# Kernel tuning notes

Hardware: AMD Instinct MI355X
Metric: run time of the kernel (lower is better)

The kernel has to match this reference:

```python
import jax, jax.numpy as jnp
import numpy as np

B, NPB, M, K, F = 4, 8192, 2048, 64, 64   # clouds, points/cloud, fps samples/cloud, max neighbors, feat dim
RADIUS = 0.2
MLP_DIMS = (F + 3, 64, 64, 128)           # local_nn: concat(x_j, pos_j - pos_i) -> 128


def setup_inputs() -> dict:
    key = jax.random.key(0)
    ks = jax.random.split(key, 8)
    N = B * NPB
    x = jax.random.normal(ks[0], (N, F), jnp.float32)
    pos = jax.random.uniform(ks[1], (N, 3), jnp.float32)  # unit cube
    batch = jnp.repeat(jnp.arange(B, dtype=jnp.int32), NPB)
    inp = {"x": x, "pos": pos, "batch": batch}
    for i in range(3):
        din, dout = MLP_DIMS[i], MLP_DIMS[i + 1]
        inp[f"W{i+1}"] = jax.random.normal(ks[2 + i], (din, dout), jnp.float32) / np.sqrt(din)
        inp[f"b{i+1}"] = jnp.zeros((dout,), jnp.float32)
    return inp


def _fps(pos_b):
    """Farthest point sampling on one cloud. pos_b: [n,3] -> [M] indices (start at point 0)."""
    d0 = jnp.sum((pos_b - pos_b[0]) ** 2, axis=-1)  # [n]
    def body(min_d, _):
        idx = jnp.argmax(min_d)
        d = jnp.sum((pos_b - pos_b[idx]) ** 2, axis=-1)
        return jnp.minimum(min_d, d), idx
    _, idxs = jax.lax.scan(body, d0, None, length=M - 1)
    return jnp.concatenate([jnp.zeros((1,), idxs.dtype), idxs])


def _sa_one_cloud(x_b, pos_b, W1, b1, W2, b2, W3, b3):
    samp = _fps(pos_b)                 # [M]
    pos_s = pos_b[samp]                # [M,3]
    # radius-ball query, capped at K nearest inside the ball (centers are in pos so self is always hit)
    d2 = jnp.sum((pos_s[:, None, :] - pos_b[None, :, :]) ** 2, axis=-1)  # [M,n]
    score = jnp.where(d2 <= RADIUS * RADIUS, -d2, -jnp.inf)
    vals, nbr = jax.lax.top_k(score, K)            # [M,K]
    valid = jnp.isfinite(vals)                     # [M,K]
    # PointConv message: MLP(concat(x_j, pos_j - pos_i)), then max-pool over neighbors
    feat = jnp.concatenate([x_b[nbr], pos_b[nbr] - pos_s[:, None, :]], axis=-1)  # [M,K,F+3]
    h = jax.nn.relu(feat @ W1 + b1)
    h = jax.nn.relu(h @ W2 + b2)
    h = jax.nn.relu(h @ W3 + b3)                   # [M,K,128]
    h = jnp.where(valid[:, :, None], h, -jnp.inf)
    return jnp.max(h, axis=1), samp                # [M,128], [M]


def reference(x, pos, batch, W1, b1, W2, b2, W3, b3):
    xb = x.reshape(B, NPB, F)
    pb = pos.reshape(B, NPB, 3)
    out, samp = jax.vmap(lambda xx, pp: _sa_one_cloud(xx, pp, W1, b1, W2, b2, W3, b3))(xb, pb)
    pos_out = jnp.take_along_axis(pb, samp[:, :, None], axis=1)       # [B,M,3]
    batch_out = jnp.repeat(jnp.arange(B, dtype=batch.dtype), M)       # [B*M]
    return out.reshape(B * M, -1), pos_out.reshape(B * M, 3), batch_out
```

## Files before the change

### kernel.cpp

```cpp
#include <hip/hip_runtime.h>

typedef unsigned int u32;
typedef unsigned long long u64;
typedef float f32x2 __attribute__((ext_vector_type(2)));

#define NPB 8192
#define BCL 4
#define MS 2048
#define KN 64
#define TOTC (BCL * MS)
#define OFF_POS   (BCL * MS * 128)
#define OFF_BATCH (OFF_POS + BCL * MS * 3)
#define SMEM_BYTES (NPB * 16 + 32 + MS * 4)
#define GRP_PRIV 40208
#define CONS_BLKS ((TOTC + 2) / 3)

__device__ inline u64 umax64(u64 a, u64 b) { return a < b ? b : a; }
__device__ inline u32 umax32(u32 a, u32 b) { return a < b ? b : a; }

__device__ inline f32x2 pk_add(f32x2 a, f32x2 b) {
  f32x2 d;
  asm("v_pk_add_f32 %0, %1, %2" : "=v"(d) : "v"(a), "v"(b));
  return d;
}
__device__ inline f32x2 pk_mul(f32x2 a, f32x2 b) {
  f32x2 d;
  asm("v_pk_mul_f32 %0, %1, %2" : "=v"(d) : "v"(a), "v"(b));
  return d;
}

__device__ inline u32 wave_max_u32(u32 v) {
  v = umax32(v, (u32)__builtin_amdgcn_update_dpp(0, (int)v, 0x111, 0xf, 0xf, false));
  v = umax32(v, (u32)__builtin_amdgcn_update_dpp(0, (int)v, 0x112, 0xf, 0xf, false));
  v = umax32(v, (u32)__builtin_amdgcn_update_dpp(0, (int)v, 0x114, 0xf, 0xf, false));
  v = umax32(v, (u32)__builtin_amdgcn_update_dpp(0, (int)v, 0x118, 0xf, 0xf, false));
  v = umax32(v, (u32)__builtin_amdgcn_update_dpp(0, (int)v, 0x142, 0xa, 0xf, false));
  v = umax32(v, (u32)__builtin_amdgcn_update_dpp(0, (int)v, 0x143, 0xc, 0xf, false));
  return (u32)__builtin_amdgcn_readlane((int)v, 63);
}
__device__ inline u64 wave_max_key(u64 lkey) {
  u32 hi = (u32)(lkey >> 32), lo32v = (u32)lkey;
  u32 m = wave_max_u32(hi);
  u32 c = wave_max_u32(hi == m ? lo32v : 0u);
  return ((u64)m << 32) | c;
}

__device__ inline u32 part1by2(u32 x) {
  x &= 0x3ffu;
  x = (x | (x << 16)) & 0x030000FFu;
  x = (x | (x << 8))  & 0x0300F00Fu;
  x = (x | (x << 4))  & 0x030C30C3u;
  x = (x | (x << 2))  & 0x09249249u;
  return x;
}

__global__ __launch_bounds__(1024) void init_ready(u32* __restrict__ ready) {
  int i = blockIdx.x * 1024 + threadIdx.x;
  if (i < TOTC) ready[i] = 0u;
}

__global__ __launch_bounds__(1024) void pipeline_kernel(
    const float* __restrict__ x, const float* __restrict__ pos,
    u32* __restrict__ ready,
    const float* __restrict__ W1, const float* __restrict__ b1,
    const float* __restrict__ W2, const float* __restrict__ b2,
    const float* __restrict__ W3, const float* __restrict__ b3,
    float* __restrict__ out) {
  __shared__ __align__(16) unsigned char smem_raw[SMEM_BYTES];
  int t = threadIdx.x;

  if (blockIdx.x < BCL) {
    u64* sortb = (u64*)smem_raw;
    float4* tab = (float4*)smem_raw;
    u64* slot = (u64*)(smem_raw + NPB * 16);
    int* s_samp = (int*)(smem_raw + NPB * 16 + 32);

    int b = blockIdx.x, lane = t & 63;
    const float* pb = pos + (size_t)b * NPB * 3;

    if (t == 1) atomicExch(&ready[(size_t)b * MS], 1u);

    for (int i = t; i < NPB; i += 1024) {
      float xx = pb[i * 3], yy = pb[i * 3 + 1], zz = pb[i * 3 + 2];
      u32 xi = (u32)fminf(fmaxf(xx * 1024.0f, 0.0f), 1023.0f);
      u32 yi = (u32)fminf(fmaxf(yy * 1024.0f, 0.0f), 1023.0f);
      u32 zi = (u32)fminf(fmaxf(zz * 1024.0f, 0.0f), 1023.0f);
      u32 m = (part1by2(zi) << 2) | (part1by2(yi) << 1) | part1by2(xi);
      sortb[i] = ((u64)m << 13) | (u32)i;
    }
    for (int k = 2; k <= NPB; k <<= 1) {
      for (int j = k >> 1; j > 0; j >>= 1) {
        __syncthreads();
        for (int i = t; i < NPB; i += 1024) {
          int ix = i ^ j;
          if (ix > i) {
            u64 a = sortb[i], c = sortb[ix];
            bool up = ((i & k) == 0);
            if ((a > c) == up) { sortb[i] = c; sortb[ix] = a; }
          }
        }
      }
    }
    __syncthreads();
    int oi[8];
    #pragma unroll
    for (int i = 0; i < 8; ++i) oi[i] = (int)(sortb[8 * t + i] & 0x1FFFu);
    __syncthreads();

    for (int i = t; i < NPB; i += 1024) {
      float xx = pb[i * 3], yy = pb[i * 3 + 1], zz = pb[i * 3 + 2];
      tab[i] = float4{xx, yy, zz, 0.0f};
    }
    if (t < 3) slot[t] = 0;
    if (t == 0) s_samp[0] = 0;
    __syncthreads();

    f32x2 px[4], py[4], pz[4], mind[4];
    u32 lo[8];
    float bxl = 1e30f, bxh = -1e30f, byl = 1e30f, byh = -1e30f, bzl = 1e30f, bzh = -1e30f;
    #pragma unroll
    for (int j = 0; j < 4; ++j) {
      int iA = oi[2 * j], iB = oi[2 * j + 1];
      float4 A = tab[iA], B = tab[iB];
      px[j] = f32x2{A.x, B.x}; py[j] = f32x2{A.y, B.y}; pz[j] = f32x2{A.z, B.z};
      lo[2 * j] = ~(u32)iA; lo[2 * j + 1] = ~(u32)iB;
      bxl = fminf(bxl, fminf(A.x, B.x)); bxh = fmaxf(bxh, fmaxf(A.x, B.x));
      byl = fminf(byl, fminf(A.y, B.y)); byh = fmaxf(byh, fmaxf(A.y, B.y));
      bzl = fminf(bzl, fminf(A.z, B.z)); bzh = fmaxf(bzh, fmaxf(A.z, B.z));
    }
    u64 lkey = 0, wkey;
    {
      float4 c0 = tab[0];
      f32x2 mcx = f32x2{-c0.x, -c0.x}, mcy = f32x2{-c0.y, -c0.y}, mcz = f32x2{-c0.z, -c0.z};
      #pragma unroll
      for (int j = 0; j < 4; ++j) {
        f32x2 dx = pk_add(px[j], mcx), dy = pk_add(py[j], mcy), dz = pk_add(pz[j], mcz);
        mind[j] = pk_add(pk_add(pk_mul(dx, dx), pk_mul(dy, dy)), pk_mul(dz, dz));
        u64 kA = ((u64)__float_as_uint(mind[j].x) << 32) | lo[2 * j];
        u64 kB = ((u64)__float_as_uint(mind[j].y) << 32) | lo[2 * j + 1];
        lkey = umax64(lkey, umax64(kA, kB));
      }
      wkey = wave_max_key(lkey);
    }

    int cur = 0, nxt = 1;
    for (int it = 1; it < MS; ++it) {
      if (lane == 0) atomicMax((u64*)&slot[cur], wkey);
      if (t == 64) slot[nxt] = 0;
      __syncthreads();
      u64 g = slot[cur];
      int win = (int)(~(u32)g) & (NPB - 1);
      if (t == 0) s_samp[it] = win;
      if (t == 65) atomicExch(&ready[(size_t)b * MS + it], (u32)(win + 1));
      float4 wc = tab[win];
      float ncx = wc.x, ncy = wc.y, ncz = wc.z;
      float lmax = __uint_as_float((u32)(lkey >> 32));
      float ax = fmaxf(fmaxf(__fsub_rn(bxl, ncx), __fsub_rn(ncx, bxh)), 0.0f);
      float ay = fmaxf(fmaxf(__fsub_rn(byl, ncy), __fsub_rn(ncy, byh)), 0.0f);
      float az = fmaxf(fmaxf(__fsub_rn(bzl, ncz), __fsub_rn(ncz, bzh)), 0.0f);
      float lb2 = (ax * ax + ay * ay + az * az) * 0.9999961853f;
      bool upd = (lb2 <= lmax);
      if (__ballot(upd)) {
        if (upd) {
          f32x2 mcx = f32x2{-ncx, -ncx}, mcy = f32x2{-ncy, -ncy}, mcz = f32x2{-ncz, -ncz};
          u64 acc = 0;
          #pragma unroll
          for (int j = 0; j < 4; ++j) {
            f32x2 dx = pk_add(px[j], mcx), dy = pk_add(py[j], mcy), dz = pk_add(pz[j], mcz);
            f32x2 d2 = pk_add(pk_add(pk_mul(dx, dx), pk_mul(dy, dy)), pk_mul(dz, dz));
            mind[j].x = fminf(mind[j].x, d2.x);
            mind[j].y = fminf(mind[j].y, d2.y);
            u64 kA = ((u64)__float_as_uint(mind[j].x) << 32) | lo[2 * j];
            u64 kB = ((u64)__float_as_uint(mind[j].y) << 32) | lo[2 * j + 1];
            acc = umax64(acc, umax64(kA, kB));
          }
          lkey = acc;
        }
        wkey = wave_max_key(lkey);
      }
      cur = nxt;
      nxt = nxt + 1 == 3 ? 0 : nxt + 1;
    }
    __syncthreads();
    float* pos_out = out + OFF_POS + (size_t)b * MS * 3;
    float* batch_out = out + OFF_BATCH + (size_t)b * MS;
    for (int m = t; m < MS; m += 1024) {
      int s = s_samp[m];
      float4 c = tab[s];
      pos_out[m * 3] = c.x;
      pos_out[m * 3 + 1] = c.y;
      pos_out[m * 3 + 2] = c.z;
      batch_out[m] = (float)b;
    }
    return;
  }

  {
    int cblk = blockIdx.x - BCL;
    int g = t >> 8;
    int tl = t & 255;
    bool work = (g < 3);
    int p = 3 * cblk + (work ? g : 0);
    if (p >= TOTC) p = TOTC - 1;
    int b = p & (BCL - 1), m = p >> 2;
    int c = b * MS + m;
    const float R2CUT = (float)(0.2 * 0.2);

    float (*s_w)[64] = (float(*)[64])(smem_raw);
    unsigned char* gb = smem_raw + 17408 + (work ? g : 0) * GRP_PRIV;
    u64* cand = (u64*)gb;
    int* s_cnt = (int*)(gb + 4096);
    int* s_win = (int*)(gb + 4100);
    float (*s_feat)[68] = (float(*)[68])(gb + 4112);
    float (*s_h)[68]    = (float(*)[68])(gb + 21520);
    float* s_mask       = (float*)(gb + 38928);
    float (*s_red)[64]  = (float(*)[64])(gb + 39184);

    const float* pb = pos + (size_t)b * NPB * 3;

    if (work && tl == 0) {
      u32 v;
      while ((v = atomicAdd(&ready[c], 0u)) == 0u) __builtin_amdgcn_s_sleep(8);
      *s_win = (int)(v - 1u);
      *s_cnt = 0;
    }
    __syncthreads();
    int s = 0;
    float cx = 0.0f, cy = 0.0f, cz = 0.0f;
    if (work) {
      s = *s_win;
      cx = pb[s * 3]; cy = pb[s * 3 + 1]; cz = pb[s * 3 + 2];
    }

    if (work) {
      for (int j = tl; j < NPB; j += 256) {
        float dx = __fsub_rn(pb[j * 3], cx);
        float dy = __fsub_rn(pb[j * 3 + 1], cy);
        float dz = __fsub_rn(pb[j * 3 + 2], cz);
        float d2 = __fadd_rn(__fadd_rn(__fmul_rn(dx, dx), __fmul_rn(dy, dy)), __fmul_rn(dz, dz));
        if (d2 <= R2CUT) {
          int sl = atomicAdd(s_cnt, 1);
          if (sl < 512) cand[sl] = ((u64)__float_as_uint(d2) << 32) | (u32)j;
        }
      }
    }
    __syncthreads();
    int n = 0;
    if (work) {
      n = *s_cnt; if (n > 512) n = 512;
      for (int i = tl; i < 512; i += 256) if (i >= n) cand[i] = ~0ull;
    }
    __syncthreads();
    for (int k = 2; k <= 512; k <<= 1) {
      for (int j = k >> 1; j > 0; j >>= 1) {
        if (work) {
          for (int i = tl; i < 512; i += 256) {
            int ix = i ^ j;
            if (ix > i) {
              u64 a = cand[i], bb = cand[ix];
              bool up = ((i & k) == 0);
              if ((a > bb) == up) { cand[i] = bb; cand[ix] = a; }
            }
          }
        }
        __syncthreads();
      }
    }

    if (work) {
      int r = tl >> 2, q = tl & 3;
      int j = (r < n) ? (int)(cand[r] & 0xffffffffu) : -1;
      bool valid = (j >= 0 && j < NPB);
      size_t jj = valid ? (size_t)j : 0;
      const float4* xp = (const float4*)(x + ((size_t)b * NPB + jj) * 64 + q * 16);
      float4 v[4];
      for (int i = 0; i < 4; ++i) v[i] = xp[i];
      for (int i = 0; i < 4; ++i) {
        s_feat[r][q * 16 + i * 4 + 0] = valid ? v[i].x : 0.0f;
        s_feat[r][q * 16 + i * 4 + 1] = valid ? v[i].y : 0.0f;
        s_feat[r][q * 16 + i * 4 + 2] = valid ? v[i].z : 0.0f;
        s_feat[r][q * 16 + i * 4 + 3] = valid ? v[i].w : 0.0f;
      }
    }
    if (work && tl < 64) {
      int r = tl;
      int j = (r < n) ? (int)(cand[r] & 0xffffffffu) : -1;
      bool valid = (j >= 0 && j < NPB);
      s_mask[r] = valid ? 0.0f : -__builtin_inff();
      size_t jj = valid ? (size_t)j : (size_t)s;
      for (int d = 0; d < 3; ++d) {
        float pj = pos[((size_t)b * NPB + jj) * 3 + d];
        float pc = pos[((size_t)b * NPB + s) * 3 + d];
        s_feat[r][64 + d] = __fsub_rn(pj, pc);
      }
    }
    for (int idx = t; idx < 67 * 64; idx += 1024)
      s_w[idx >> 6][idx & 63] = W1[idx];
    __syncthreads();

    {
      int r = tl >> 2, n0 = (tl & 3) * 16;
      float acc[16];
      if (work) {
        for (int j = 0; j < 16; ++j) acc[j] = b1[n0 + j];
        for (int k = 0; k < 67; ++k) {
          float f = s_feat[r][k];
          for (int j = 0; j < 16; ++j) acc[j] += f * s_w[k][n0 + j];
        }
      }
      __syncthreads();
      if (work) {
        for (int j = 0; j < 16; ++j) s_h[r][n0 + j] = fmaxf(acc[j], 0.0f);
      }
      for (int idx = t; idx < 64 * 64; idx += 1024)
        s_w[idx >> 6][idx & 63] = W2[idx];
    }
    __syncthreads();

    {
      int r = tl >> 2, n0 = (tl & 3) * 16;
      float acc[16];
      if (work) {
        for (int j = 0; j < 16; ++j) acc[j] = b2[n0 + j];
        for (int k = 0; k < 64; ++k) {
          float f = s_h[r][k];
          for (int j = 0; j < 16; ++j) acc[j] += f * s_w[k][n0 + j];
        }
      }
      __syncthreads();
      if (work) {
        for (int j = 0; j < 16; ++j) s_feat[r][n0 + j] = fmaxf(acc[j], 0.0f);
      }
    }
    __syncthreads();

    for (int h = 0; h < 2; ++h) {
      for (int idx = t; idx < 64 * 64; idx += 1024)
        s_w[idx >> 6][idx & 63] = W3[(size_t)(idx >> 6) * 128 + h * 64 + (idx & 63)];
      __syncthreads();
      if (work) {
        int n2 = tl & 63, rg = tl >> 6;
        float acc[16];
        float bias = b3[h * 64 + n2];
        for (int rr = 0; rr < 16; ++rr) acc[rr] = bias;
        for (int k = 0; k < 64; ++k) {
          float w = s_w[k][n2];
          for (int rr = 0; rr < 16; ++rr) acc[rr] += s_feat[rg * 16 + rr][k] * w;
        }
        float mm = -__builtin_inff();
        for (int rr = 0; rr < 16; ++rr)
          mm = fmaxf(mm, fmaxf(acc[rr], 0.0f) + s_mask[rg * 16 + rr]);
        s_red[rg][n2] = mm;
      }
      __syncthreads();
      if (work && tl < 64) {
        float mm = fmaxf(fmaxf(s_red[0][tl], s_red[1][tl]), fmaxf(s_red[2][tl], s_red[3][tl]));
        out[(size_t)c * 128 + h * 64 + tl] = mm;
      }
      __syncthreads();
    }
  }
}

extern "C" void kernel_launch(void* const* d_in, const int* in_sizes, int n_in,
                              void* d_out, int out_size, void* d_ws, size_t ws_size,
                              hipStream_t stream) {
  const float* x   = (const float*)d_in[0];
  const float* pos = (const float*)d_in[1];
  const float* W1 = (const float*)d_in[3];
  const float* b1 = (const float*)d_in[4];
  const float* W2 = (const float*)d_in[5];
  const float* b2 = (const float*)d_in[6];
  const float* W3 = (const float*)d_in[7];
  const float* b3 = (const float*)d_in[8];

  float* out = (float*)d_out;
  u32* ready = (u32*)d_ws;

  init_ready<<<(TOTC + 1023) / 1024, 1024, 0, stream>>>(ready);
  pipeline_kernel<<<BCL + CONS_BLKS, 1024, 0, stream>>>(
      x, pos, ready, W1, b1, W2, b2, W3, b3, out);
}
```

Measured before the change: 1.484 ms.

## Spread FPS argmax atomics over four LDS slots and batch ready-flag publishes

The per-iteration LDS atomicMax used to hit one slot from all 16 waves. It now spreads across four slots that are reduced after the barrier, which cuts same-address atomic serialization on the FPS critical path. The producer also packs four 13-bit sample indices into one 64-bit ready word with a valid bit, so it issues a global atomic only every fourth iteration. In exchange, consumers see samples up to three iterations later, which slightly delays pipeline overlap.

```diff
diff --git a/kernel.cpp b/kernel.cpp
--- a/kernel.cpp
+++ b/kernel.cpp
@@ -11,7 +11,7 @@
 #define TOTC (BCL * MS)
 #define OFF_POS   (BCL * MS * 128)
 #define OFF_BATCH (OFF_POS + BCL * MS * 3)
-#define SMEM_BYTES (NPB * 16 + 32 + MS * 4)
+#define SMEM_BYTES (NPB * 16 + 96 + MS * 4)
 #define GRP_PRIV 40208
 #define CONS_BLKS ((TOTC + 2) / 3)
 
@@ -54,14 +54,14 @@
   return x;
 }
 
-__global__ __launch_bounds__(1024) void init_ready(u32* __restrict__ ready) {
+__global__ __launch_bounds__(1024) void init_ready(u64* __restrict__ ready) {
   int i = blockIdx.x * 1024 + threadIdx.x;
-  if (i < TOTC) ready[i] = 0u;
+  if (i < TOTC / 4) ready[i] = 0ull;
 }
 
 __global__ __launch_bounds__(1024) void pipeline_kernel(
     const float* __restrict__ x, const float* __restrict__ pos,
-    u32* __restrict__ ready,
+    u64* __restrict__ ready,
     const float* __restrict__ W1, const float* __restrict__ b1,
     const float* __restrict__ W2, const float* __restrict__ b2,
     const float* __restrict__ W3, const float* __restrict__ b3,
@@ -72,13 +72,11 @@
   if (blockIdx.x < BCL) {
     u64* sortb = (u64*)smem_raw;
     float4* tab = (float4*)smem_raw;
-    u64* slot = (u64*)(smem_raw + NPB * 16);
-    int* s_samp = (int*)(smem_raw + NPB * 16 + 32);
-
-    int b = blockIdx.x, lane = t & 63;
+    u64 (*slotv)[4] = (u64(*)[4])(smem_raw + NPB * 16);
+    int* s_samp = (int*)(smem_raw + NPB * 16 + 96);
+
+    int b = blockIdx.x, lane = t & 63, wid = t >> 6;
     const float* pb = pos + (size_t)b * NPB * 3;
-
-    if (t == 1) atomicExch(&ready[(size_t)b * MS], 1u);
 
     for (int i = t; i < NPB; i += 1024) {
       float xx = pb[i * 3], yy = pb[i * 3 + 1], zz = pb[i * 3 + 2];
@@ -111,7 +109,7 @@
       float xx = pb[i * 3], yy = pb[i * 3 + 1], zz = pb[i * 3 + 2];
       tab[i] = float4{xx, yy, zz, 0.0f};
     }
-    if (t < 3) slot[t] = 0;
+    if (t < 12) ((u64*)slotv)[t] = 0;
     if (t == 0) s_samp[0] = 0;
     __syncthreads();
 
@@ -143,15 +141,23 @@
       wkey = wave_max_key(lkey);
     }
 
+    u64 pk = 0;
     int cur = 0, nxt = 1;
     for (int it = 1; it < MS; ++it) {
-      if (lane == 0) atomicMax((u64*)&slot[cur], wkey);
-      if (t == 64) slot[nxt] = 0;
-      __syncthreads();
-      u64 g = slot[cur];
+      if (lane == 0) atomicMax(&slotv[cur][wid & 3], wkey);
+      if (t >= 64 && t < 68) slotv[nxt][t - 64] = 0;
+      __syncthreads();
+      ulonglong2 s01 = *(const ulonglong2*)&slotv[cur][0];
+      ulonglong2 s23 = *(const ulonglong2*)&slotv[cur][2];
+      u64 g = umax64(umax64(s01.x, s01.y), umax64(s23.x, s23.y));
       int win = (int)(~(u32)g) & (NPB - 1);
       if (t == 0) s_samp[it] = win;
-      if (t == 65) atomicExch(&ready[(size_t)b * MS + it], (u32)(win + 1));
+      pk = (pk << 13) | (u32)win;
+      if ((it & 3) == 3) {
+        if (t == 65)
+          atomicExch(&ready[(size_t)b * (MS / 4) + (it >> 2)], pk | (1ull << 63));
+        pk = 0;
+      }
       float4 wc = tab[win];
       float ncx = wc.x, ncy = wc.y, ncz = wc.z;
       float lmax = __uint_as_float((u32)(lkey >> 32));
@@ -219,9 +225,11 @@
     const float* pb = pos + (size_t)b * NPB * 3;
 
     if (work && tl == 0) {
-      u32 v;
-      while ((v = atomicAdd(&ready[c], 0u)) == 0u) __builtin_amdgcn_s_sleep(8);
-      *s_win = (int)(v - 1u);
+      int grp = m >> 2, sub = m & 3;
+      u64 v;
+      while (!((v = atomicAdd(&ready[(size_t)b * (MS / 4) + grp], 0ull)) >> 63))
+        __builtin_amdgcn_s_sleep(8);
+      *s_win = (int)((v >> ((3 - sub) * 13)) & (u64)(NPB - 1));
       *s_cnt = 0;
     }
     __syncthreads();
@@ -375,9 +383,9 @@
   const float* b3 = (const float*)d_in[8];
 
   float* out = (float*)d_out;
-  u32* ready = (u32*)d_ws;
-
-  init_ready<<<(TOTC + 1023) / 1024, 1024, 0, stream>>>(ready);
+  u64* ready = (u64*)d_ws;
+
+  init_ready<<<(TOTC / 4 + 1023) / 1024, 1024, 0, stream>>>(ready);
   pipeline_kernel<<<BCL + CONS_BLKS, 1024, 0, stream>>>(
       x, pos, ready, W1, b1, W2, b2, W3, b3, out);
 }
```

Measured after the change: 1.775 ms. +19.6%, slower.

## Map four clouds' centers per consumer block and relax FPS barrier

Applied to the files above, without the earlier changes.

Consumer blocks now handle one sample index across all four clouds, one 256-thread group per cloud, instead of three centers per block with an idle fourth group. Because producers advance all clouds in lockstep, each block's four centers become ready at about the same time. The separate hidden-layer buffer is dropped in favour of writing layer outputs back in place into the feature buffer, which shrinks per-group shared memory so four groups fit. The FPS loop swaps __syncthreads for an explicit lgkmcnt wait plus s_barrier with a scheduling barrier, aiming to cut per-iteration sync cost; this relies on the LDS/scalar waitcnt being enough for correctness.

```diff
diff --git a/kernel.cpp b/kernel.cpp
--- a/kernel.cpp
+++ b/kernel.cpp
@@ -12,8 +12,8 @@
 #define OFF_POS   (BCL * MS * 128)
 #define OFF_BATCH (OFF_POS + BCL * MS * 3)
 #define SMEM_BYTES (NPB * 16 + 32 + MS * 4)
-#define GRP_PRIV 40208
-#define CONS_BLKS ((TOTC + 2) / 3)
+#define GRP_PRIV 22800
+#define CONS_BLKS MS
 
 __device__ inline u64 umax64(u64 a, u64 b) { return a < b ? b : a; }
 __device__ inline u32 umax32(u32 a, u32 b) { return a < b ? b : a; }
@@ -147,7 +147,9 @@
     for (int it = 1; it < MS; ++it) {
       if (lane == 0) atomicMax((u64*)&slot[cur], wkey);
       if (t == 64) slot[nxt] = 0;
-      __syncthreads();
+      asm volatile("s_waitcnt lgkmcnt(0)" ::: "memory");
+      __builtin_amdgcn_s_barrier();
+      __builtin_amdgcn_sched_barrier(0);
       u64 g = slot[cur];
       int win = (int)(~(u32)g) & (NPB - 1);
       if (t == 0) s_samp[it] = win;
@@ -199,75 +201,60 @@
     int cblk = blockIdx.x - BCL;
     int g = t >> 8;
     int tl = t & 255;
-    bool work = (g < 3);
-    int p = 3 * cblk + (work ? g : 0);
-    if (p >= TOTC) p = TOTC - 1;
-    int b = p & (BCL - 1), m = p >> 2;
+    int b = g, m = cblk;
     int c = b * MS + m;
     const float R2CUT = (float)(0.2 * 0.2);
 
     float (*s_w)[64] = (float(*)[64])(smem_raw);
-    unsigned char* gb = smem_raw + 17408 + (work ? g : 0) * GRP_PRIV;
+    unsigned char* gb = smem_raw + 17408 + g * GRP_PRIV;
     u64* cand = (u64*)gb;
     int* s_cnt = (int*)(gb + 4096);
     int* s_win = (int*)(gb + 4100);
     float (*s_feat)[68] = (float(*)[68])(gb + 4112);
-    float (*s_h)[68]    = (float(*)[68])(gb + 21520);
-    float* s_mask       = (float*)(gb + 38928);
-    float (*s_red)[64]  = (float(*)[64])(gb + 39184);
+    float* s_mask       = (float*)(gb + 21520);
+    float (*s_red)[64]  = (float(*)[64])(gb + 21776);
 
     const float* pb = pos + (size_t)b * NPB * 3;
 
-    if (work && tl == 0) {
+    if (tl == 0) {
       u32 v;
       while ((v = atomicAdd(&ready[c], 0u)) == 0u) __builtin_amdgcn_s_sleep(8);
       *s_win = (int)(v - 1u);
       *s_cnt = 0;
     }
     __syncthreads();
-    int s = 0;
-    float cx = 0.0f, cy = 0.0f, cz = 0.0f;
-    if (work) {
-      s = *s_win;
-      cx = pb[s * 3]; cy = pb[s * 3 + 1]; cz = pb[s * 3 + 2];
-    }
-
-    if (work) {
-      for (int j = tl; j < NPB; j += 256) {
-        float dx = __fsub_rn(pb[j * 3], cx);
-        float dy = __fsub_rn(pb[j * 3 + 1], cy);
-        float dz = __fsub_rn(pb[j * 3 + 2], cz);
-        float d2 = __fadd_rn(__fadd_rn(__fmul_rn(dx, dx), __fmul_rn(dy, dy)), __fmul_rn(dz, dz));
-        if (d2 <= R2CUT) {
-          int sl = atomicAdd(s_cnt, 1);
-          if (sl < 512) cand[sl] = ((u64)__float_as_uint(d2) << 32) | (u32)j;
-        }
-      }
-    }
-    __syncthreads();
-    int n = 0;
-    if (work) {
-      n = *s_cnt; if (n > 512) n = 512;
-      for (int i = tl; i < 512; i += 256) if (i >= n) cand[i] = ~0ull;
-    }
+    int s = *s_win;
+    float cx = pb[s * 3], cy = pb[s * 3 + 1], cz = pb[s * 3 + 2];
+
+    for (int j = tl; j < NPB; j += 256) {
+      float dx = __fsub_rn(pb[j * 3], cx);
+      float dy = __fsub_rn(pb[j * 3 + 1], cy);
+      float dz = __fsub_rn(pb[j * 3 + 2], cz);
+      float d2 = __fadd_rn(__fadd_rn(__fmul_rn(dx, dx), __fmul_rn(dy, dy)), __fmul_rn(dz, dz));
+      if (d2 <= R2CUT) {
+        int sl = atomicAdd(s_cnt, 1);
+        if (sl < 512) cand[sl] = ((u64)__float_as_uint(d2) << 32) | (u32)j;
+      }
+    }
+    __syncthreads();
+    int n = *s_cnt; if (n > 512) n = 512;
+    for (int i = tl; i < 512; i += 256) if (i >= n) cand[i] = ~0ull;
     __syncthreads();
     for (int k = 2; k <= 512; k <<= 1) {
       for (int j = k >> 1; j > 0; j >>= 1) {
-        if (work) {
-          for (int i = tl; i < 512; i += 256) {
-            int ix = i ^ j;
-            if (ix > i) {
-              u64 a = cand[i], bb = cand[ix];
-              bool up = ((i & k) == 0);
-              if ((a > bb) == up) { cand[i] = bb; cand[ix] = a; }
-            }
+        for (int i = tl; i < 512; i += 256) {
+          int ix = i ^ j;
+          if (ix > i) {
+            u64 a = cand[i], bb = cand[ix];
+            bool up = ((i & k) == 0);
+            if ((a > bb) == up) { cand[i] = bb; cand[ix] = a; }
           }
         }
         __syncthreads();
       }
     }
 
-    if (work) {
+    {
       int r = tl >> 2, q = tl & 3;
       int j = (r < n) ? (int)(cand[r] & 0xffffffffu) : -1;
       bool valid = (j >= 0 && j < NPB);
@@ -282,7 +269,7 @@
         s_feat[r][q * 16 + i * 4 + 3] = valid ? v[i].w : 0.0f;
       }
     }
-    if (work && tl < 64) {
+    if (tl < 64) {
       int r = tl;
       int j = (r < n) ? (int)(cand[r] & 0xffffffffu) : -1;
       bool valid = (j >= 0 && j < NPB);
@@ -301,17 +288,13 @@
     {
       int r = tl >> 2, n0 = (tl & 3) * 16;
       float acc[16];
-      if (work) {
-        for (int j = 0; j < 16; ++j) acc[j] = b1[n0 + j];
-        for (int k = 0; k < 67; ++k) {
-          float f = s_feat[r][k];
-          for (int j = 0; j < 16; ++j) acc[j] += f * s_w[k][n0 + j];
-        }
-      }
-      __syncthreads();
-      if (work) {
-        for (int j = 0; j < 16; ++j) s_h[r][n0 + j] = fmaxf(acc[j], 0.0f);
-      }
+      for (int j = 0; j < 16; ++j) acc[j] = b1[n0 + j];
+      for (int k = 0; k < 67; ++k) {
+        float f = s_feat[r][k];
+        for (int j = 0; j < 16; ++j) acc[j] += f * s_w[k][n0 + j];
+      }
+      __syncthreads();
+      for (int j = 0; j < 16; ++j) s_feat[r][n0 + j] = fmaxf(acc[j], 0.0f);
       for (int idx = t; idx < 64 * 64; idx += 1024)
         s_w[idx >> 6][idx & 63] = W2[idx];
     }
@@ -320,17 +303,13 @@
     {
       int r = tl >> 2, n0 = (tl & 3) * 16;
       float acc[16];
-      if (work) {
-        for (int j = 0; j < 16; ++j) acc[j] = b2[n0 + j];
-        for (int k = 0; k < 64; ++k) {
-          float f = s_h[r][k];
-          for (int j = 0; j < 16; ++j) acc[j] += f * s_w[k][n0 + j];
-        }
-      }
-      __syncthreads();
-      if (work) {
-        for (int j = 0; j < 16; ++j) s_feat[r][n0 + j] = fmaxf(acc[j], 0.0f);
-      }
+      for (int j = 0; j < 16; ++j) acc[j] = b2[n0 + j];
+      for (int k = 0; k < 64; ++k) {
+        float f = s_feat[r][k];
+        for (int j = 0; j < 16; ++j) acc[j] += f * s_w[k][n0 + j];
+      }
+      __syncthreads();
+      for (int j = 0; j < 16; ++j) s_feat[r][n0 + j] = fmaxf(acc[j], 0.0f);
     }
     __syncthreads();
 
@@ -338,24 +317,22 @@
       for (int idx = t; idx < 64 * 64; idx += 1024)
         s_w[idx >> 6][idx & 63] = W3[(size_t)(idx >> 6) * 128 + h * 64 + (idx & 63)];
       __syncthreads();
-      if (work) {
-        int n2 = tl & 63, rg = tl >> 6;
-        float acc[16];
-        float bias = b3[h * 64 + n2];
-        for (int rr = 0; rr < 16; ++rr) acc[rr] = bias;
-        for (int k = 0; k < 64; ++k) {
-          float w = s_w[k][n2];
-          for (int rr = 0; rr < 16; ++rr) acc[rr] += s_feat[rg * 16 + rr][k] * w;
-        }
-        float mm = -__builtin_inff();
-        for (int rr = 0; rr < 16; ++rr)
-          mm = fmaxf(mm, fmaxf(acc[rr], 0.0f) + s_mask[rg * 16 + rr]);
-        s_red[rg][n2] = mm;
-      }
-      __syncthreads();
-      if (work && tl < 64) {
-        float mm = fmaxf(fmaxf(s_red[0][tl], s_red[1][tl]), fmaxf(s_red[2][tl], s_red[3][tl]));
-        out[(size_t)c * 128 + h * 64 + tl] = mm;
+      int n2 = tl & 63, rg = tl >> 6;
+      float acc[16];
+      float bias = b3[h * 64 + n2];
+      for (int rr = 0; rr < 16; ++rr) acc[rr] = bias;
+      for (int k = 0; k < 64; ++k) {
+        float w = s_w[k][n2];
+        for (int rr = 0; rr < 16; ++rr) acc[rr] += s_feat[rg * 16 + rr][k] * w;
+      }
+      float mm = -__builtin_inff();
+      for (int rr = 0; rr < 16; ++rr)
+        mm = fmaxf(mm, fmaxf(acc[rr], 0.0f) + s_mask[rg * 16 + rr]);
+      s_red[rg][n2] = mm;
+      __syncthreads();
+      if (tl < 64) {
+        float mm2 = fmaxf(fmaxf(s_red[0][tl], s_red[1][tl]), fmaxf(s_red[2][tl], s_red[3][tl]));
+        out[(size_t)c * 128 + h * 64 + tl] = mm2;
       }
       __syncthreads();
     }
```

New measurement: 1.495 ms. Within noise of the previous version (+0.7%).

## Use persistent consumer blocks with cloud positions cached in LDS

Applied to the files above, without the earlier changes.

Consumer blocks become persistent: each block is bound to one cloud, copies that cloud's positions into shared memory once, and loops over 17 centers in a strided slot order, with two working groups per block instead of three. The ball query and relative-position computation now read the LDS copy instead of global memory. The intermediate s_h buffer is dropped in favour of writing back into s_feat, and the FPS barrier becomes a raw s_barrier with an explicit lgkmcnt wait. This is meant to cut repeated global position reads and block launch overhead, but it lowers per-block parallelism and lets consumers sit spinning while they wait on FPS progress.

```diff
diff --git a/kernel.cpp b/kernel.cpp
--- a/kernel.cpp
+++ b/kernel.cpp
@@ -11,9 +11,14 @@
 #define TOTC (BCL * MS)
 #define OFF_POS   (BCL * MS * 128)
 #define OFF_BATCH (OFF_POS + BCL * MS * 3)
-#define SMEM_BYTES (NPB * 16 + 32 + MS * 4)
-#define GRP_PRIV 40208
-#define CONS_BLKS ((TOTC + 2) / 3)
+#define TAB3_B   98304
+#define SW_OFF   98304
+#define GRP_OFF  115712
+#define GRP_PRIV 22800
+#define SMEM_BYTES 161312
+#define CONS_BLKS 252
+#define SLOTS 126
+#define NITER 17
 
 __device__ inline u64 umax64(u64 a, u64 b) { return a < b ? b : a; }
 __device__ inline u32 umax32(u32 a, u32 b) { return a < b ? b : a; }
@@ -147,7 +152,9 @@
     for (int it = 1; it < MS; ++it) {
       if (lane == 0) atomicMax((u64*)&slot[cur], wkey);
       if (t == 64) slot[nxt] = 0;
-      __syncthreads();
+      asm volatile("s_waitcnt lgkmcnt(0)" ::: "memory");
+      __builtin_amdgcn_s_barrier();
+      __builtin_amdgcn_sched_barrier(0);
       u64 g = slot[cur];
       int win = (int)(~(u32)g) & (NPB - 1);
       if (t == 0) s_samp[it] = win;
@@ -196,168 +203,177 @@
   }
 
   {
-    int cblk = blockIdx.x - BCL;
+    int cb = blockIdx.x - BCL;
+    int b = cb & (BCL - 1);
+    int q = cb >> 2;
     int g = t >> 8;
     int tl = t & 255;
-    bool work = (g < 3);
-    int p = 3 * cblk + (work ? g : 0);
-    if (p >= TOTC) p = TOTC - 1;
-    int b = p & (BCL - 1), m = p >> 2;
-    int c = b * MS + m;
+    bool work = (g < 2);
+    int slot = q * 2 + (work ? g : 0);
     const float R2CUT = (float)(0.2 * 0.2);
 
-    float (*s_w)[64] = (float(*)[64])(smem_raw);
-    unsigned char* gb = smem_raw + 17408 + (work ? g : 0) * GRP_PRIV;
+    float* tab3 = (float*)smem_raw;
+    float (*s_w)[64] = (float(*)[64])(smem_raw + SW_OFF);
+    unsigned char* gb = smem_raw + GRP_OFF + (work ? g : 0) * GRP_PRIV;
     u64* cand = (u64*)gb;
     int* s_cnt = (int*)(gb + 4096);
     int* s_win = (int*)(gb + 4100);
     float (*s_feat)[68] = (float(*)[68])(gb + 4112);
-    float (*s_h)[68]    = (float(*)[68])(gb + 21520);
-    float* s_mask       = (float*)(gb + 38928);
-    float (*s_red)[64]  = (float(*)[64])(gb + 39184);
+    float* s_mask       = (float*)(gb + 21520);
+    float (*s_red)[64]  = (float(*)[64])(gb + 21776);
 
     const float* pb = pos + (size_t)b * NPB * 3;
-
-    if (work && tl == 0) {
-      u32 v;
-      while ((v = atomicAdd(&ready[c], 0u)) == 0u) __builtin_amdgcn_s_sleep(8);
-      *s_win = (int)(v - 1u);
-      *s_cnt = 0;
-    }
-    __syncthreads();
-    int s = 0;
-    float cx = 0.0f, cy = 0.0f, cz = 0.0f;
-    if (work) {
-      s = *s_win;
-      cx = pb[s * 3]; cy = pb[s * 3 + 1]; cz = pb[s * 3 + 2];
-    }
-
-    if (work) {
-      for (int j = tl; j < NPB; j += 256) {
-        float dx = __fsub_rn(pb[j * 3], cx);
-        float dy = __fsub_rn(pb[j * 3 + 1], cy);
-        float dz = __fsub_rn(pb[j * 3 + 2], cz);
-        float d2 = __fadd_rn(__fadd_rn(__fmul_rn(dx, dx), __fmul_rn(dy, dy)), __fmul_rn(dz, dz));
-        if (d2 <= R2CUT) {
-          int sl = atomicAdd(s_cnt, 1);
-          if (sl < 512) cand[sl] = ((u64)__float_as_uint(d2) << 32) | (u32)j;
-        }
-      }
-    }
-    __syncthreads();
-    int n = 0;
-    if (work) {
-      n = *s_cnt; if (n > 512) n = 512;
-      for (int i = tl; i < 512; i += 256) if (i >= n) cand[i] = ~0ull;
-    }
-    __syncthreads();
-    for (int k = 2; k <= 512; k <<= 1) {
-      for (int j = k >> 1; j > 0; j >>= 1) {
-        if (work) {
-          for (int i = tl; i < 512; i += 256) {
-            int ix = i ^ j;
-            if (ix > i) {
-              u64 a = cand[i], bb = cand[ix];
-              bool up = ((i & k) == 0);
-              if ((a > bb) == up) { cand[i] = bb; cand[ix] = a; }
+    for (int i = t; i < NPB * 3; i += 1024) tab3[i] = pb[i];
+    __syncthreads();
+
+    for (int k = 0; k < NITER; ++k) {
+      int m = slot + k * SLOTS;
+      if (m >= MS) m = MS - 1;
+      int c = b * MS + m;
+
+      if (work && tl == 0) {
+        u32 v;
+        while ((v = __hip_atomic_load(&ready[c], __ATOMIC_RELAXED,
+                                      __HIP_MEMORY_SCOPE_AGENT)) == 0u)
+          __builtin_amdgcn_s_sleep(32);
+        *s_win = (int)(v - 1u);
+        *s_cnt = 0;
+      }
+      __syncthreads();
+      int s = 0;
+      float cx = 0.0f, cy = 0.0f, cz = 0.0f;
+      if (work) {
+        s = *s_win;
+        cx = tab3[s * 3]; cy = tab3[s * 3 + 1]; cz = tab3[s * 3 + 2];
+      }
+
+      if (work) {
+        for (int j = tl; j < NPB; j += 256) {
+          float dx = __fsub_rn(tab3[j * 3], cx);
+          float dy = __fsub_rn(tab3[j * 3 + 1], cy);
+          float dz = __fsub_rn(tab3[j * 3 + 2], cz);
+          float d2 = __fadd_rn(__fadd_rn(__fmul_rn(dx, dx), __fmul_rn(dy, dy)), __fmul_rn(dz, dz));
+          if (d2 <= R2CUT) {
+            int sl = atomicAdd(s_cnt, 1);
+            if (sl < 512) cand[sl] = ((u64)__float_as_uint(d2) << 32) | (u32)j;
+          }
+        }
+      }
+      __syncthreads();
+      int n = 0;
+      if (work) {
+        n = *s_cnt; if (n > 512) n = 512;
+        for (int i = tl; i < 512; i += 256) if (i >= n) cand[i] = ~0ull;
+      }
+      __syncthreads();
+      for (int kk = 2; kk <= 512; kk <<= 1) {
+        for (int j = kk >> 1; j > 0; j >>= 1) {
+          if (work) {
+            for (int i = tl; i < 512; i += 256) {
+              int ix = i ^ j;
+              if (ix > i) {
+                u64 a = cand[i], bb = cand[ix];
+                bool up = ((i & kk) == 0);
+                if ((a > bb) == up) { cand[i] = bb; cand[ix] = a; }
+              }
             }
           }
-        }
-        __syncthreads();
-      }
-    }
-
-    if (work) {
-      int r = tl >> 2, q = tl & 3;
-      int j = (r < n) ? (int)(cand[r] & 0xffffffffu) : -1;
-      bool valid = (j >= 0 && j < NPB);
-      size_t jj = valid ? (size_t)j : 0;
-      const float4* xp = (const float4*)(x + ((size_t)b * NPB + jj) * 64 + q * 16);
-      float4 v[4];
-      for (int i = 0; i < 4; ++i) v[i] = xp[i];
-      for (int i = 0; i < 4; ++i) {
-        s_feat[r][q * 16 + i * 4 + 0] = valid ? v[i].x : 0.0f;
-        s_feat[r][q * 16 + i * 4 + 1] = valid ? v[i].y : 0.0f;
-        s_feat[r][q * 16 + i * 4 + 2] = valid ? v[i].z : 0.0f;
-        s_feat[r][q * 16 + i * 4 + 3] = valid ? v[i].w : 0.0f;
-      }
-    }
-    if (work && tl < 64) {
-      int r = tl;
-      int j = (r < n) ? (int)(cand[r] & 0xffffffffu) : -1;
-      bool valid = (j >= 0 && j < NPB);
-      s_mask[r] = valid ? 0.0f : -__builtin_inff();
-      size_t jj = valid ? (size_t)j : (size_t)s;
-      for (int d = 0; d < 3; ++d) {
-        float pj = pos[((size_t)b * NPB + jj) * 3 + d];
-        float pc = pos[((size_t)b * NPB + s) * 3 + d];
-        s_feat[r][64 + d] = __fsub_rn(pj, pc);
-      }
-    }
-    for (int idx = t; idx < 67 * 64; idx += 1024)
-      s_w[idx >> 6][idx & 63] = W1[idx];
-    __syncthreads();
-
-    {
-      int r = tl >> 2, n0 = (tl & 3) * 16;
-      float acc[16];
+          __syncthreads();
+        }
+      }
+
       if (work) {
-        for (int j = 0; j < 16; ++j) acc[j] = b1[n0 + j];
-        for (int k = 0; k < 67; ++k) {
-          float f = s_feat[r][k];
-          for (int j = 0; j < 16; ++j) acc[j] += f * s_w[k][n0 + j];
-        }
-      }
-      __syncthreads();
-      if (work) {
-        for (int j = 0; j < 16; ++j) s_h[r][n0 + j] = fmaxf(acc[j], 0.0f);
-      }
-      for (int idx = t; idx < 64 * 64; idx += 1024)
-        s_w[idx >> 6][idx & 63] = W2[idx];
-    }
-    __syncthreads();
-
-    {
-      int r = tl >> 2, n0 = (tl & 3) * 16;
-      float acc[16];
-      if (work) {
-        for (int j = 0; j < 16; ++j) acc[j] = b2[n0 + j];
-        for (int k = 0; k < 64; ++k) {
-          float f = s_h[r][k];
-          for (int j = 0; j < 16; ++j) acc[j] += f * s_w[k][n0 + j];
-        }
-      }
-      __syncthreads();
-      if (work) {
-        for (int j = 0; j < 16; ++j) s_feat[r][n0 + j] = fmaxf(acc[j], 0.0f);
-      }
-    }
-    __syncthreads();
-
-    for (int h = 0; h < 2; ++h) {
-      for (int idx = t; idx < 64 * 64; idx += 1024)
-        s_w[idx >> 6][idx & 63] = W3[(size_t)(idx >> 6) * 128 + h * 64 + (idx & 63)];
-      __syncthreads();
-      if (work) {
-        int n2 = tl & 63, rg = tl >> 6;
+        int r = tl >> 2, qq = tl & 3;
+        int j = (r < n) ? (int)(cand[r] & 0xffffffffu) : -1;
+        bool valid = (j >= 0 && j < NPB);
+        size_t jj = valid ? (size_t)j : 0;
+        const float4* xp = (const float4*)(x + ((size_t)b * NPB + jj) * 64 + qq * 16);
+        float4 v[4];
+        for (int i = 0; i < 4; ++i) v[i] = xp[i];
+        for (int i = 0; i < 4; ++i) {
+          s_feat[r][qq * 16 + i * 4 + 0] = valid ? v[i].x : 0.0f;
+          s_feat[r][qq * 16 + i * 4 + 1] = valid ? v[i].y : 0.0f;
+          s_feat[r][qq * 16 + i * 4 + 2] = valid ? v[i].z : 0.0f;
+          s_feat[r][qq * 16 + i * 4 + 3] = valid ? v[i].w : 0.0f;
+        }
+      }
+      if (work && tl < 64) {
+        int r = tl;
+        int j = (r < n) ? (int)(cand[r] & 0xffffffffu) : -1;
+        bool valid = (j >= 0 && j < NPB);
+        s_mask[r] = valid ? 0.0f : -__builtin_inff();
+        size_t jj = valid ? (size_t)j : (size_t)s;
+        for (int d = 0; d < 3; ++d) {
+          float pj = tab3[jj * 3 + d];
+          float pc = tab3[(size_t)s * 3 + d];
+          s_feat[r][64 + d] = __fsub_rn(pj, pc);
+        }
+      }
+      for (int idx = t; idx < 67 * 64; idx += 1024)
+        s_w[idx >> 6][idx & 63] = W1[idx];
+      __syncthreads();
+
+      {
+        int r = tl >> 2, n0 = (tl & 3) * 16;
         float acc[16];
-        float bias = b3[h * 64 + n2];
-        for (int rr = 0; rr < 16; ++rr) acc[rr] = bias;
-        for (int k = 0; k < 64; ++k) {
-          float w = s_w[k][n2];
-          for (int rr = 0; rr < 16; ++rr) acc[rr] += s_feat[rg * 16 + rr][k] * w;
-        }
-        float mm = -__builtin_inff();
-        for (int rr = 0; rr < 16; ++rr)
-          mm = fmaxf(mm, fmaxf(acc[rr], 0.0f) + s_mask[rg * 16 + rr]);
-        s_red[rg][n2] = mm;
-      }
-      __syncthreads();
-      if (work && tl < 64) {
-        float mm = fmaxf(fmaxf(s_red[0][tl], s_red[1][tl]), fmaxf(s_red[2][tl], s_red[3][tl]));
-        out[(size_t)c * 128 + h * 64 + tl] = mm;
-      }
-      __syncthreads();
+        if (work) {
+          for (int j = 0; j < 16; ++j) acc[j] = b1[n0 + j];
+          for (int kk = 0; kk < 67; ++kk) {
+            float f = s_feat[r][kk];
+            for (int j = 0; j < 16; ++j) acc[j] += f * s_w[kk][n0 + j];
+          }
+        }
+        __syncthreads();
+        if (work) {
+          for (int j = 0; j < 16; ++j) s_feat[r][n0 + j] = fmaxf(acc[j], 0.0f);
+        }
+        for (int idx = t; idx < 64 * 64; idx += 1024)
+          s_w[idx >> 6][idx & 63] = W2[idx];
+      }
+      __syncthreads();
+
+      {
+        int r = tl >> 2, n0 = (tl & 3) * 16;
+        float acc[16];
+        if (work) {
+          for (int j = 0; j < 16; ++j) acc[j] = b2[n0 + j];
+          for (int kk = 0; kk < 64; ++kk) {
+            float f = s_feat[r][kk];
+            for (int j = 0; j < 16; ++j) acc[j] += f * s_w[kk][n0 + j];
+          }
+        }
+        __syncthreads();
+        if (work) {
+          for (int j = 0; j < 16; ++j) s_feat[r][n0 + j] = fmaxf(acc[j], 0.0f);
+        }
+      }
+      __syncthreads();
+
+      for (int h = 0; h < 2; ++h) {
+        for (int idx = t; idx < 64 * 64; idx += 1024)
+          s_w[idx >> 6][idx & 63] = W3[(size_t)(idx >> 6) * 128 + h * 64 + (idx & 63)];
+        __syncthreads();
+        if (work) {
+          int n2 = tl & 63, rg = tl >> 6;
+          float acc[16];
+          float bias = b3[h * 64 + n2];
+          for (int rr = 0; rr < 16; ++rr) acc[rr] = bias;
+          for (int kk = 0; kk < 64; ++kk) {
+            float w = s_w[kk][n2];
+            for (int rr = 0; rr < 16; ++rr) acc[rr] += s_feat[rg * 16 + rr][kk] * w;
+          }
+          float mm = -__builtin_inff();
+          for (int rr = 0; rr < 16; ++rr)
+            mm = fmaxf(mm, fmaxf(acc[rr], 0.0f) + s_mask[rg * 16 + rr]);
+          s_red[rg][n2] = mm;
+        }
+        __syncthreads();
+        if (work && tl < 64) {
+          float mm2 = fmaxf(fmaxf(s_red[0][tl], s_red[1][tl]), fmaxf(s_red[2][tl], s_red[3][tl]));
+          out[(size_t)c * 128 + h * 64 + tl] = mm2;
+        }
+        __syncthreads();
+      }
     }
   }
 }
```

Measured after the change: 1.582 ms. 6.6% more time.
